# Optimization experiments

Hardware: AMD Instinct MI355X
Metric: run time of the kernel (lower is better)

Reference implementation:

```python
import jax, jax.numpy as jnp
import numpy as np

N_EMBD = 1024
BLOCK_SIZE = 128
HEAD_SIZE = 128
THETA = 10000.0


def setup_inputs() -> dict:
    key = jax.random.key(0)
    k1, k2, k3, k4 = jax.random.split(key, 4)
    B, T = 256, BLOCK_SIZE
    x = jax.random.normal(k1, (B, T, N_EMBD), dtype=jnp.float32)
    # nn.Linear(n_embd, head_size, bias=False) stored as [n_embd, head_size] so y = x @ W
    s = 1.0 / np.sqrt(N_EMBD)
    Wq = jax.random.normal(k2, (N_EMBD, HEAD_SIZE), dtype=jnp.float32) * s
    Wk = jax.random.normal(k3, (N_EMBD, HEAD_SIZE), dtype=jnp.float32) * s
    Wv = jax.random.normal(k4, (N_EMBD, HEAD_SIZE), dtype=jnp.float32) * s
    return {"x": x, "Wq": Wq, "Wk": Wk, "Wv": Wv}


def _rope_cos_sin(T: int, head_size: int):
    # freqs = exp(arange(0, hs, 2) * (-log(theta)/hs)); angles = outer(t, freqs)
    inv_freq = jnp.exp(jnp.arange(0, head_size, 2, dtype=jnp.float32) * (-np.log(THETA) / head_size))
    angles = jnp.arange(T, dtype=jnp.float32)[:, None] * inv_freq[None, :]  # [T, hs/2]
    return jnp.cos(angles), jnp.sin(angles)


def _apply_rope(t, cos, sin):
    # complex-view rotation on interleaved (even, odd) pairs of the last dim
    tr = t[..., 0::2]  # real parts  [B,T,hs/2]
    ti = t[..., 1::2]  # imag parts
    out_r = tr * cos - ti * sin
    out_i = tr * sin + ti * cos
    return jnp.stack([out_r, out_i], axis=-1).reshape(t.shape)


def reference(x, Wq, Wk, Wv):
    B, T, _ = x.shape
    hs = Wq.shape[1]
    q = x @ Wq  # [B,T,hs]
    k = x @ Wk
    v = x @ Wv
    cos, sin = _rope_cos_sin(T, hs)
    q = _apply_rope(q, cos, sin)
    k = _apply_rope(k, cos, sin)
    scores = jnp.einsum('btd,bsd->bts', q, k) / jnp.sqrt(jnp.asarray(hs, q.dtype))
    causal = jnp.tril(jnp.ones((T, T), dtype=bool))
    scores = jnp.where(causal[None, :, :], scores, -jnp.inf)
    att = jax.nn.softmax(scores, axis=-1)  # dropout is identity in eval
    return jnp.einsum('bts,bsd->btd', att, v)
```

## Files before the change

kernel.cpp:

```cpp
#include <hip/hip_runtime.h>
#include <math.h>

typedef __bf16 bf16x8 __attribute__((ext_vector_type(8)));
typedef float  f32x4  __attribute__((ext_vector_type(4)));
typedef unsigned short us4 __attribute__((ext_vector_type(4)));

constexpr int N_EMBD = 1024;
constexpr int T_SEQ  = 128;
constexpr int HS     = 128;
constexpr int BATCH  = 256;
constexpr int ROWS   = BATCH * T_SEQ;

__device__ __forceinline__ void async16(const void* g, void* l) {
    __builtin_amdgcn_global_load_lds(
        (const __attribute__((address_space(1))) unsigned int*)g,
        (__attribute__((address_space(3))) unsigned int*)l, 16, 0, 0);
}
__device__ __forceinline__ unsigned short bfbits(float f) {
    return __builtin_bit_cast(unsigned short, (__bf16)f);
}
__device__ __forceinline__ f32x4 zero4() {
    f32x4 z = {0.f, 0.f, 0.f, 0.f};
    return z;
}

__global__ __launch_bounds__(256) void wcast(
    const float* __restrict__ Wq, const float* __restrict__ Wk,
    const float* __restrict__ Wv, unsigned short* __restrict__ Wt)
{
    __shared__ unsigned short tile[64][130];
    const int bid = blockIdx.x;
    const int nt  = bid >> 4;
    const int k0  = (bid & 15) << 6;
    const float* src = (nt == 0) ? Wq : ((nt == 1) ? Wk : Wv);
    const int tid = threadIdx.x;
#pragma unroll
    for (int j = 0; j < 32; ++j) {
        int idx = tid + j * 256;
        int k = idx >> 7, n = idx & 127;
        tile[k][n] = bfbits(src[(size_t)(k0 + k) * HS + n]);
    }
    __syncthreads();
#pragma unroll
    for (int j = 0; j < 32; ++j) {
        int idx = tid + j * 256;
        int n = idx >> 6, kk = idx & 63;
        Wt[(size_t)(nt * 128 + n) * N_EMBD + k0 + kk] = tile[kk][n];
    }
}

__global__ __launch_bounds__(512, 4) void qkv_gemm(
    const float* __restrict__ x,
    const unsigned short* __restrict__ Wt,
    unsigned short* __restrict__ qb,
    unsigned short* __restrict__ kb,
    unsigned short* __restrict__ vt)
{
    __shared__ char lds[65536];
    const int tid = threadIdx.x;
    const int w  = tid >> 6;
    const int l  = tid & 63;
    const int cl = l & 15;
    const int quad = l >> 4;
    const int mt  = blockIdx.x;
    const int row0 = mt << 6;
    const int wm0 = (w & 1) << 5;
    const int wn0 = (w >> 1) * 96;

    f32x4 acc[2][6];
#pragma unroll
    for (int a = 0; a < 2; ++a)
#pragma unroll
        for (int b = 0; b < 6; ++b) acc[a][b] = zero4();

    for (int kc = 0; kc < N_EMBD; kc += 64) {
        __syncthreads();
#pragma unroll
        for (int jj = 0; jj < 2; ++jj) {
            int j = w * 2 + jj;
            int m = j * 4 + (l >> 4);
            int csrc = (l & 15) ^ (m & 15);
            async16(x + (size_t)(row0 + m) * N_EMBD + kc + csrc * 4, lds + j * 1024);
        }
#pragma unroll
        for (int jj = 0; jj < 6; ++jj) {
            int j = w * 6 + jj;
            int n = j * 8 + (l >> 3);
            int csrc = (l & 7) ^ (l >> 3);
            async16(Wt + (size_t)n * N_EMBD + kc + csrc * 8, lds + 16384 + j * 1024);
        }
        __syncthreads();

#pragma unroll
        for (int ks = 0; ks < 2; ++ks) {
            const int kq = ks * 4 + quad;
            bf16x8 af[2], bf[6];
#pragma unroll
            for (int rt = 0; rt < 2; ++rt) {
                int m = wm0 + rt * 16 + cl;
                int c0 = kq * 2;
                f32x4 a0 = *(const f32x4*)(lds + ((m * 16 + (c0 ^ cl)) << 4));
                f32x4 a1 = *(const f32x4*)(lds + ((m * 16 + ((c0 + 1) ^ cl)) << 4));
                bf16x8 t;
                t[0] = (__bf16)a0[0]; t[1] = (__bf16)a0[1];
                t[2] = (__bf16)a0[2]; t[3] = (__bf16)a0[3];
                t[4] = (__bf16)a1[0]; t[5] = (__bf16)a1[1];
                t[6] = (__bf16)a1[2]; t[7] = (__bf16)a1[3];
                af[rt] = t;
            }
#pragma unroll
            for (int ct = 0; ct < 6; ++ct) {
                int n = wn0 + ct * 16 + cl;
                bf[ct] = *(const bf16x8*)(lds + 16384 + ((n * 8 + (kq ^ (l & 7))) << 4));
            }
#pragma unroll
            for (int rt = 0; rt < 2; ++rt)
#pragma unroll
                for (int ct = 0; ct < 6; ++ct)
                    acc[rt][ct] = __builtin_amdgcn_mfma_f32_16x16x32_bf16(
                        af[rt], bf[ct], acc[rt][ct], 0, 0, 0);
        }
    }

    const float LNT = 0.07195578430905272f;
    const int bidx = row0 >> 7;
    const int srow0 = row0 & 127;
#pragma unroll
    for (int ct = 0; ct < 6; ++ct) {
        int c  = wn0 + ct * 16 + cl;
        int ntc = c >> 7;
        int d  = c & 127;
        if (ntc < 2) {
            unsigned short* dst = (ntc == 0) ? qb : kb;
            float freq = __expf(-(float)(d & ~1) * LNT);
#pragma unroll
            for (int rt = 0; rt < 2; ++rt) {
#pragma unroll
                for (int i = 0; i < 4; ++i) {
                    int grow = row0 + wm0 + rt * 16 + quad * 4 + i;
                    int t = grow & 127;
                    float v = acc[rt][ct][i];
                    float p = __shfl_xor(v, 1);
                    float sn, cs;
                    __sincosf((float)t * freq, &sn, &cs);
                    float r = ((d & 1) == 0) ? (v * cs - p * sn) : (p * sn + v * cs);
                    dst[(size_t)grow * HS + d] = bfbits(r);
                }
            }
        } else {
#pragma unroll
            for (int rt = 0; rt < 2; ++rt) {
                int s0 = srow0 + wm0 + rt * 16 + quad * 4;
                us4 u;
                u.x = bfbits(acc[rt][ct][0]);
                u.y = bfbits(acc[rt][ct][1]);
                u.z = bfbits(acc[rt][ct][2]);
                u.w = bfbits(acc[rt][ct][3]);
                *(us4*)(vt + (size_t)bidx * 16384 + d * 128 + s0) = u;
            }
        }
    }
}

__global__ __launch_bounds__(64) void attn(
    const unsigned short* __restrict__ qb,
    const unsigned short* __restrict__ kb,
    const unsigned short* __restrict__ vt,
    float* __restrict__ out)
{
    __shared__ char plds[16 * 272];
    const int l = threadIdx.x;
    const int cl = l & 15;
    const int quad = l >> 4;
    const int b  = blockIdx.x >> 3;
    const int rg = blockIdx.x & 7;
    const int nct = rg + 1;
    const int nks = (rg + 2) >> 1;

    const unsigned short* qB = qb + (size_t)b * 16384;
    const unsigned short* kB = kb + (size_t)b * 16384;
    const unsigned short* vB = vt + (size_t)b * 16384;

    bf16x8 af[4];
#pragma unroll
    for (int ks = 0; ks < 4; ++ks)
        af[ks] = *(const bf16x8*)(qB + (size_t)(rg * 16 + cl) * HS + (ks * 4 + quad) * 8);

    f32x4 s[8];
#pragma unroll
    for (int ct = 0; ct < 8; ++ct) s[ct] = zero4();

#pragma unroll
    for (int ct = 0; ct < 8; ++ct) if (ct < nct) {
        const unsigned short* kr = kB + (size_t)(ct * 16 + cl) * HS;
#pragma unroll
        for (int ks = 0; ks < 4; ++ks) {
            bf16x8 bb = *(const bf16x8*)(kr + (ks * 4 + quad) * 8);
            s[ct] = __builtin_amdgcn_mfma_f32_16x16x32_bf16(af[ks], bb, s[ct], 0, 0, 0);
        }
    }

    const float scale = 0.08838834764831845f;
#pragma unroll
    for (int i = 0; i < 4; ++i) {
        int t = rg * 16 + quad * 4 + i;
        float mx = -3.0e38f;
#pragma unroll
        for (int ct = 0; ct < 8; ++ct) if (ct < nct) {
            int col = ct * 16 + cl;
            float v = s[ct][i] * scale;
            v = (col <= t) ? v : -INFINITY;
            s[ct][i] = v;
            mx = fmaxf(mx, v);
        }
        mx = fmaxf(mx, __shfl_xor(mx, 1));
        mx = fmaxf(mx, __shfl_xor(mx, 2));
        mx = fmaxf(mx, __shfl_xor(mx, 4));
        mx = fmaxf(mx, __shfl_xor(mx, 8));
        float sum = 0.f;
#pragma unroll
        for (int ct = 0; ct < 8; ++ct) if (ct < nct) {
            float p = __expf(s[ct][i] - mx);
            s[ct][i] = p;
            sum += p;
        }
        sum += __shfl_xor(sum, 1);
        sum += __shfl_xor(sum, 2);
        sum += __shfl_xor(sum, 4);
        sum += __shfl_xor(sum, 8);
        float inv = 1.0f / sum;
        int rl = quad * 4 + i;
#pragma unroll
        for (int ct = 0; ct < 8; ++ct) if (ct < nct) {
            *(unsigned short*)(plds + rl * 272 + (ct * 16 + cl) * 2) =
                bfbits(s[ct][i] * inv);
        }
    }
    if ((rg & 1) == 0) {
#pragma unroll
        for (int i = 0; i < 4; ++i)
            *(unsigned short*)(plds + (quad * 4 + i) * 272 + (nct * 16 + cl) * 2) = 0;
    }

    bf16x8 ap[4];
#pragma unroll
    for (int ks = 0; ks < 4; ++ks) if (ks < nks)
        ap[ks] = *(const bf16x8*)(plds + cl * 272 + (ks * 4 + quad) * 16);

    f32x4 o[8];
#pragma unroll
    for (int ct = 0; ct < 8; ++ct) o[ct] = zero4();

#pragma unroll
    for (int ct = 0; ct < 8; ++ct) {
        const unsigned short* vr = vB + (size_t)(ct * 16 + cl) * 128;
#pragma unroll
        for (int ks = 0; ks < 4; ++ks) if (ks < nks) {
            bf16x8 bb = *(const bf16x8*)(vr + (ks * 4 + quad) * 8);
            o[ct] = __builtin_amdgcn_mfma_f32_16x16x32_bf16(ap[ks], bb, o[ct], 0, 0, 0);
        }
    }

#pragma unroll
    for (int ct = 0; ct < 8; ++ct)
#pragma unroll
        for (int i = 0; i < 4; ++i) {
            int t = rg * 16 + quad * 4 + i;
            out[(size_t)b * 16384 + (size_t)t * HS + ct * 16 + cl] = o[ct][i];
        }
}

extern "C" void kernel_launch(void* const* d_in, const int* in_sizes, int n_in,
                              void* d_out, int out_size, void* d_ws, size_t ws_size,
                              hipStream_t stream) {
    const float* x  = (const float*)d_in[0];
    const float* Wq = (const float*)d_in[1];
    const float* Wk = (const float*)d_in[2];
    const float* Wv = (const float*)d_in[3];
    float* out = (float*)d_out;

    unsigned short* qb = (unsigned short*)d_ws;
    unsigned short* kb = qb + (size_t)ROWS * HS;
    unsigned short* vt = kb + (size_t)ROWS * HS;
    unsigned short* Wt = vt + (size_t)ROWS * HS;

    wcast<<<48, 256, 0, stream>>>(Wq, Wk, Wv, Wt);
    qkv_gemm<<<512, 512, 0, stream>>>(x, Wt, qb, kb, vt);
    attn<<<2048, 64, 0, stream>>>(qb, kb, vt, out);
}
```

Measured before the change: 250.4 us.

## Register-prefetch x as bf16 into LDS, widen GEMM warp tiles, specialize attention per row group

The QKV GEMM now runs 256 threads per block, and each warp computes a 64x96 tile, which doubles A-fragment reuse per warp. Activations are loaded from global into registers one K-chunk ahead, converted to bf16 once, and stored into a swizzled bf16 LDS tile. This halves the A footprint in LDS and removes the repeated fp32-to-bf16 conversion each warp used to do. The attention kernel is templated on the row group, so loop bounds are compile-time constants and the register arrays shrink. The cost is more accumulator registers per thread (24 f32x4) and fewer warps per block, which may lower occupancy.

```diff
diff --git a/kernel.cpp b/kernel.cpp
--- a/kernel.cpp
+++ b/kernel.cpp
@@ -49,72 +49,84 @@
     }
 }
 
-__global__ __launch_bounds__(512, 4) void qkv_gemm(
+__global__ __launch_bounds__(256, 2) void qkv_gemm(
     const float* __restrict__ x,
     const unsigned short* __restrict__ Wt,
     unsigned short* __restrict__ qb,
     unsigned short* __restrict__ kb,
     unsigned short* __restrict__ vt)
 {
-    __shared__ char lds[65536];
+    __shared__ char lds[57344];
     const int tid = threadIdx.x;
     const int w  = tid >> 6;
     const int l  = tid & 63;
     const int cl = l & 15;
     const int quad = l >> 4;
-    const int mt  = blockIdx.x;
-    const int row0 = mt << 6;
-    const int wm0 = (w & 1) << 5;
-    const int wn0 = (w >> 1) * 96;
-
-    f32x4 acc[2][6];
-#pragma unroll
-    for (int a = 0; a < 2; ++a)
+    const int row0 = blockIdx.x << 6;
+    const int wn0 = w * 96;
+
+    const int ar = tid >> 2;
+    const int ac = tid & 3;
+    const int aslot0 = (ac * 2) ^ (ar & 7);
+    const int aslot1 = (ac * 2 + 1) ^ (ar & 7);
+    const float* aptr = x + (size_t)(row0 + ar) * N_EMBD + ac * 16;
+
+    f32x4 acc[4][6];
+#pragma unroll
+    for (int a = 0; a < 4; ++a)
 #pragma unroll
         for (int b = 0; b < 6; ++b) acc[a][b] = zero4();
+
+    f32x4 ar0 = *(const f32x4*)(aptr);
+    f32x4 ar1 = *(const f32x4*)(aptr + 4);
+    f32x4 ar2 = *(const f32x4*)(aptr + 8);
+    f32x4 ar3 = *(const f32x4*)(aptr + 12);
 
     for (int kc = 0; kc < N_EMBD; kc += 64) {
         __syncthreads();
-#pragma unroll
-        for (int jj = 0; jj < 2; ++jj) {
-            int j = w * 2 + jj;
-            int m = j * 4 + (l >> 4);
-            int csrc = (l & 15) ^ (m & 15);
-            async16(x + (size_t)(row0 + m) * N_EMBD + kc + csrc * 4, lds + j * 1024);
-        }
-#pragma unroll
-        for (int jj = 0; jj < 6; ++jj) {
-            int j = w * 6 + jj;
+        bf16x8 w0, w1;
+        w0[0] = (__bf16)ar0[0]; w0[1] = (__bf16)ar0[1];
+        w0[2] = (__bf16)ar0[2]; w0[3] = (__bf16)ar0[3];
+        w0[4] = (__bf16)ar1[0]; w0[5] = (__bf16)ar1[1];
+        w0[6] = (__bf16)ar1[2]; w0[7] = (__bf16)ar1[3];
+        w1[0] = (__bf16)ar2[0]; w1[1] = (__bf16)ar2[1];
+        w1[2] = (__bf16)ar2[2]; w1[3] = (__bf16)ar2[3];
+        w1[4] = (__bf16)ar3[0]; w1[5] = (__bf16)ar3[1];
+        w1[6] = (__bf16)ar3[2]; w1[7] = (__bf16)ar3[3];
+        *(bf16x8*)(lds + ar * 128 + aslot0 * 16) = w0;
+        *(bf16x8*)(lds + ar * 128 + aslot1 * 16) = w1;
+#pragma unroll
+        for (int jj = 0; jj < 12; ++jj) {
+            int j = w * 12 + jj;
             int n = j * 8 + (l >> 3);
             int csrc = (l & 7) ^ (l >> 3);
-            async16(Wt + (size_t)n * N_EMBD + kc + csrc * 8, lds + 16384 + j * 1024);
+            async16(Wt + (size_t)n * N_EMBD + kc + csrc * 8, lds + 8192 + j * 1024);
         }
         __syncthreads();
 
+        if (kc + 64 < N_EMBD) {
+            const float* ap2 = aptr + kc + 64;
+            ar0 = *(const f32x4*)(ap2);
+            ar1 = *(const f32x4*)(ap2 + 4);
+            ar2 = *(const f32x4*)(ap2 + 8);
+            ar3 = *(const f32x4*)(ap2 + 12);
+        }
+
 #pragma unroll
         for (int ks = 0; ks < 2; ++ks) {
-            const int kq = ks * 4 + quad;
-            bf16x8 af[2], bf[6];
-#pragma unroll
-            for (int rt = 0; rt < 2; ++rt) {
-                int m = wm0 + rt * 16 + cl;
-                int c0 = kq * 2;
-                f32x4 a0 = *(const f32x4*)(lds + ((m * 16 + (c0 ^ cl)) << 4));
-                f32x4 a1 = *(const f32x4*)(lds + ((m * 16 + ((c0 + 1) ^ cl)) << 4));
-                bf16x8 t;
-                t[0] = (__bf16)a0[0]; t[1] = (__bf16)a0[1];
-                t[2] = (__bf16)a0[2]; t[3] = (__bf16)a0[3];
-                t[4] = (__bf16)a1[0]; t[5] = (__bf16)a1[1];
-                t[6] = (__bf16)a1[2]; t[7] = (__bf16)a1[3];
-                af[rt] = t;
+            bf16x8 af[4], bf[6];
+#pragma unroll
+            for (int rt = 0; rt < 4; ++rt) {
+                int m = rt * 16 + cl;
+                af[rt] = *(const bf16x8*)(lds + m * 128 + (((ks * 4 + quad) ^ (m & 7)) << 4));
             }
 #pragma unroll
             for (int ct = 0; ct < 6; ++ct) {
                 int n = wn0 + ct * 16 + cl;
-                bf[ct] = *(const bf16x8*)(lds + 16384 + ((n * 8 + (kq ^ (l & 7))) << 4));
+                bf[ct] = *(const bf16x8*)(lds + 8192 + n * 128 + (((ks * 4 + quad) ^ (n & 7)) << 4));
             }
 #pragma unroll
-            for (int rt = 0; rt < 2; ++rt)
+            for (int rt = 0; rt < 4; ++rt)
 #pragma unroll
                 for (int ct = 0; ct < 6; ++ct)
                     acc[rt][ct] = __builtin_amdgcn_mfma_f32_16x16x32_bf16(
@@ -134,10 +146,10 @@
             unsigned short* dst = (ntc == 0) ? qb : kb;
             float freq = __expf(-(float)(d & ~1) * LNT);
 #pragma unroll
-            for (int rt = 0; rt < 2; ++rt) {
+            for (int rt = 0; rt < 4; ++rt) {
 #pragma unroll
                 for (int i = 0; i < 4; ++i) {
-                    int grow = row0 + wm0 + rt * 16 + quad * 4 + i;
+                    int grow = row0 + rt * 16 + quad * 4 + i;
                     int t = grow & 127;
                     float v = acc[rt][ct][i];
                     float p = __shfl_xor(v, 1);
@@ -149,8 +161,8 @@
             }
         } else {
 #pragma unroll
-            for (int rt = 0; rt < 2; ++rt) {
-                int s0 = srow0 + wm0 + rt * 16 + quad * 4;
+            for (int rt = 0; rt < 4; ++rt) {
+                int s0 = srow0 + rt * 16 + quad * 4;
                 us4 u;
                 u.x = bfbits(acc[rt][ct][0]);
                 u.y = bfbits(acc[rt][ct][1]);
@@ -160,6 +172,105 @@
             }
         }
     }
+}
+
+template<int RG>
+__device__ __forceinline__ void attn_body(
+    const unsigned short* __restrict__ qB,
+    const unsigned short* __restrict__ kB,
+    const unsigned short* __restrict__ vB,
+    float* __restrict__ outB, char* plds, int l)
+{
+    constexpr int NCT = RG + 1;
+    constexpr int NKS = (RG + 2) >> 1;
+    const int cl = l & 15;
+    const int quad = l >> 4;
+
+    bf16x8 af[4];
+#pragma unroll
+    for (int ks = 0; ks < 4; ++ks)
+        af[ks] = *(const bf16x8*)(qB + (size_t)(RG * 16 + cl) * HS + (ks * 4 + quad) * 8);
+
+    f32x4 s[NCT];
+#pragma unroll
+    for (int ct = 0; ct < NCT; ++ct) s[ct] = zero4();
+
+#pragma unroll
+    for (int ct = 0; ct < NCT; ++ct) {
+        const unsigned short* kr = kB + (size_t)(ct * 16 + cl) * HS;
+#pragma unroll
+        for (int ks = 0; ks < 4; ++ks) {
+            bf16x8 bb = *(const bf16x8*)(kr + (ks * 4 + quad) * 8);
+            s[ct] = __builtin_amdgcn_mfma_f32_16x16x32_bf16(af[ks], bb, s[ct], 0, 0, 0);
+        }
+    }
+
+    const float scale = 0.08838834764831845f;
+#pragma unroll
+    for (int i = 0; i < 4; ++i) {
+        int t = RG * 16 + quad * 4 + i;
+        float mx = -3.0e38f;
+#pragma unroll
+        for (int ct = 0; ct < NCT; ++ct) {
+            int col = ct * 16 + cl;
+            float v = s[ct][i] * scale;
+            v = (col <= t) ? v : -INFINITY;
+            s[ct][i] = v;
+            mx = fmaxf(mx, v);
+        }
+        mx = fmaxf(mx, __shfl_xor(mx, 1));
+        mx = fmaxf(mx, __shfl_xor(mx, 2));
+        mx = fmaxf(mx, __shfl_xor(mx, 4));
+        mx = fmaxf(mx, __shfl_xor(mx, 8));
+        float sum = 0.f;
+#pragma unroll
+        for (int ct = 0; ct < NCT; ++ct) {
+            float p = __expf(s[ct][i] - mx);
+            s[ct][i] = p;
+            sum += p;
+        }
+        sum += __shfl_xor(sum, 1);
+        sum += __shfl_xor(sum, 2);
+        sum += __shfl_xor(sum, 4);
+        sum += __shfl_xor(sum, 8);
+        float inv = 1.0f / sum;
+        int rl = quad * 4 + i;
+#pragma unroll
+        for (int ct = 0; ct < NCT; ++ct) {
+            *(unsigned short*)(plds + rl * 272 + (ct * 16 + cl) * 2) =
+                bfbits(s[ct][i] * inv);
+        }
+        if ((RG & 1) == 0) {
+            *(unsigned short*)(plds + rl * 272 + (NCT * 16 + cl) * 2) = 0;
+        }
+    }
+
+    bf16x8 ap[NKS];
+#pragma unroll
+    for (int ks = 0; ks < NKS; ++ks)
+        ap[ks] = *(const bf16x8*)(plds + cl * 272 + (ks * 4 + quad) * 16);
+
+    f32x4 o[8];
+#pragma unroll
+    for (int ct = 0; ct < 8; ++ct) o[ct] = zero4();
+
+#pragma unroll
+    for (int ct = 0; ct < 8; ++ct) {
+        const unsigned short* vr = vB + (size_t)(ct * 16 + cl) * 128;
+#pragma unroll
+        for (int ks = 0; ks < NKS; ++ks) {
+            bf16x8 bb = *(const bf16x8*)(vr + (ks * 4 + quad) * 8);
+            o[ct] = __builtin_amdgcn_mfma_f32_16x16x32_bf16(ap[ks], bb, o[ct], 0, 0, 0);
+        }
+    }
+
+#pragma unroll
+    for (int ct = 0; ct < 8; ++ct)
+#pragma unroll
+        for (int i = 0; i < 4; ++i) {
+            int t = RG * 16 + quad * 4 + i;
+            outB[(size_t)t * HS + ct * 16 + cl] = o[ct][i];
+        }
 }
 
 __global__ __launch_bounds__(64) void attn(
@@ -170,104 +281,24 @@
 {
     __shared__ char plds[16 * 272];
     const int l = threadIdx.x;
-    const int cl = l & 15;
-    const int quad = l >> 4;
     const int b  = blockIdx.x >> 3;
     const int rg = blockIdx.x & 7;
-    const int nct = rg + 1;
-    const int nks = (rg + 2) >> 1;
 
     const unsigned short* qB = qb + (size_t)b * 16384;
     const unsigned short* kB = kb + (size_t)b * 16384;
     const unsigned short* vB = vt + (size_t)b * 16384;
-
-    bf16x8 af[4];
-#pragma unroll
-    for (int ks = 0; ks < 4; ++ks)
-        af[ks] = *(const bf16x8*)(qB + (size_t)(rg * 16 + cl) * HS + (ks * 4 + quad) * 8);
-
-    f32x4 s[8];
-#pragma unroll
-    for (int ct = 0; ct < 8; ++ct) s[ct] = zero4();
-
-#pragma unroll
-    for (int ct = 0; ct < 8; ++ct) if (ct < nct) {
-        const unsigned short* kr = kB + (size_t)(ct * 16 + cl) * HS;
-#pragma unroll
-        for (int ks = 0; ks < 4; ++ks) {
-            bf16x8 bb = *(const bf16x8*)(kr + (ks * 4 + quad) * 8);
-            s[ct] = __builtin_amdgcn_mfma_f32_16x16x32_bf16(af[ks], bb, s[ct], 0, 0, 0);
-        }
-    }
-
-    const float scale = 0.08838834764831845f;
-#pragma unroll
-    for (int i = 0; i < 4; ++i) {
-        int t = rg * 16 + quad * 4 + i;
-        float mx = -3.0e38f;
-#pragma unroll
-        for (int ct = 0; ct < 8; ++ct) if (ct < nct) {
-            int col = ct * 16 + cl;
-            float v = s[ct][i] * scale;
-            v = (col <= t) ? v : -INFINITY;
-            s[ct][i] = v;
-            mx = fmaxf(mx, v);
-        }
-        mx = fmaxf(mx, __shfl_xor(mx, 1));
-        mx = fmaxf(mx, __shfl_xor(mx, 2));
-        mx = fmaxf(mx, __shfl_xor(mx, 4));
-        mx = fmaxf(mx, __shfl_xor(mx, 8));
-        float sum = 0.f;
-#pragma unroll
-        for (int ct = 0; ct < 8; ++ct) if (ct < nct) {
-            float p = __expf(s[ct][i] - mx);
-            s[ct][i] = p;
-            sum += p;
-        }
-        sum += __shfl_xor(sum, 1);
-        sum += __shfl_xor(sum, 2);
-        sum += __shfl_xor(sum, 4);
-        sum += __shfl_xor(sum, 8);
-        float inv = 1.0f / sum;
-        int rl = quad * 4 + i;
-#pragma unroll
-        for (int ct = 0; ct < 8; ++ct) if (ct < nct) {
-            *(unsigned short*)(plds + rl * 272 + (ct * 16 + cl) * 2) =
-                bfbits(s[ct][i] * inv);
-        }
-    }
-    if ((rg & 1) == 0) {
-#pragma unroll
-        for (int i = 0; i < 4; ++i)
-            *(unsigned short*)(plds + (quad * 4 + i) * 272 + (nct * 16 + cl) * 2) = 0;
-    }
-
-    bf16x8 ap[4];
-#pragma unroll
-    for (int ks = 0; ks < 4; ++ks) if (ks < nks)
-        ap[ks] = *(const bf16x8*)(plds + cl * 272 + (ks * 4 + quad) * 16);
-
-    f32x4 o[8];
-#pragma unroll
-    for (int ct = 0; ct < 8; ++ct) o[ct] = zero4();
-
-#pragma unroll
-    for (int ct = 0; ct < 8; ++ct) {
-        const unsigned short* vr = vB + (size_t)(ct * 16 + cl) * 128;
-#pragma unroll
-        for (int ks = 0; ks < 4; ++ks) if (ks < nks) {
-            bf16x8 bb = *(const bf16x8*)(vr + (ks * 4 + quad) * 8);
-            o[ct] = __builtin_amdgcn_mfma_f32_16x16x32_bf16(ap[ks], bb, o[ct], 0, 0, 0);
-        }
-    }
-
-#pragma unroll
-    for (int ct = 0; ct < 8; ++ct)
-#pragma unroll
-        for (int i = 0; i < 4; ++i) {
-            int t = rg * 16 + quad * 4 + i;
-            out[(size_t)b * 16384 + (size_t)t * HS + ct * 16 + cl] = o[ct][i];
-        }
+    float* outB = out + (size_t)b * 16384;
+
+    switch (rg) {
+        case 0: attn_body<0>(qB, kB, vB, outB, plds, l); break;
+        case 1: attn_body<1>(qB, kB, vB, outB, plds, l); break;
+        case 2: attn_body<2>(qB, kB, vB, outB, plds, l); break;
+        case 3: attn_body<3>(qB, kB, vB, outB, plds, l); break;
+        case 4: attn_body<4>(qB, kB, vB, outB, plds, l); break;
+        case 5: attn_body<5>(qB, kB, vB, outB, plds, l); break;
+        case 6: attn_body<6>(qB, kB, vB, outB, plds, l); break;
+        default: attn_body<7>(qB, kB, vB, outB, plds, l); break;
+    }
 }
 
 extern "C" void kernel_launch(void* const* d_in, const int* in_sizes, int n_in,
@@ -285,6 +316,6 @@
     unsigned short* Wt = vt + (size_t)ROWS * HS;
 
     wcast<<<48, 256, 0, stream>>>(Wq, Wk, Wv, Wt);
-    qkv_gemm<<<512, 512, 0, stream>>>(x, Wt, qb, kb, vt);
+    qkv_gemm<<<512, 256, 0, stream>>>(x, Wt, qb, kb, vt);
     attn<<<2048, 64, 0, stream>>>(qb, kb, vt, out);
 }
```

Result: faster. 240.1 us (-4.1%).

## Fuse QKV projection, RoPE and causal attention into one per-batch kernel

Applied to the files above, without the earlier changes.

Replaces the separate QKV GEMM and attention kernels with one kernel that handles one batch element per 512-thread block. The block projects x to Q, K and V, applies RoPE, keeps Q, K and V^T in LDS, and each wave computes attention for 16 query rows. This removes the global-memory round trip for bf16 Q, K and V and one kernel launch. The GEMM also changes its staging: x is prefetched into registers, converted to bf16 and stored in LDS with a K step of 32. The cost is roughly 139KB of LDS per block and only 256 blocks, so each CU runs a single block and there is less occupancy to hide the latency of reading x.

```diff
diff --git a/kernel.cpp b/kernel.cpp
--- a/kernel.cpp
+++ b/kernel.cpp
@@ -49,142 +49,126 @@
     }
 }
 
-__global__ __launch_bounds__(512, 4) void qkv_gemm(
+__global__ __launch_bounds__(512, 2) void head_fused(
     const float* __restrict__ x,
     const unsigned short* __restrict__ Wt,
-    unsigned short* __restrict__ qb,
-    unsigned short* __restrict__ kb,
-    unsigned short* __restrict__ vt)
+    float* __restrict__ out)
 {
-    __shared__ char lds[65536];
-    const int tid = threadIdx.x;
-    const int w  = tid >> 6;
-    const int l  = tid & 63;
-    const int cl = l & 15;
+    __shared__ char lds[139264];
+    constexpr int QS = 0;
+    constexpr int KS = 34816;
+    constexpr int VS = 69632;
+    constexpr int STG_A = 104448;
+    constexpr int STG_B = 114688;
+
+    const int tid  = threadIdx.x;
+    const int w    = tid >> 6;
+    const int l    = tid & 63;
+    const int cl   = l & 15;
     const int quad = l >> 4;
-    const int mt  = blockIdx.x;
-    const int row0 = mt << 6;
-    const int wm0 = (w & 1) << 5;
-    const int wn0 = (w >> 1) * 96;
-
-    f32x4 acc[2][6];
-#pragma unroll
-    for (int a = 0; a < 2; ++a)
-#pragma unroll
-        for (int b = 0; b < 6; ++b) acc[a][b] = zero4();
-
-    for (int kc = 0; kc < N_EMBD; kc += 64) {
+    const int b    = blockIdx.x;
+    const int row0 = b << 7;
+    const int wm   = (w & 1) << 6;
+    const int wn   = (w >> 1) * 96;
+
+    const int arow = tid >> 2;
+    const int acol = (tid & 3) << 3;
+    const float* aptr = x + (size_t)(row0 + arow) * N_EMBD + acol;
+    const int bsrc = (l & 3) ^ quad;
+
+    f32x4 acc[4][6];
+#pragma unroll
+    for (int a = 0; a < 4; ++a)
+#pragma unroll
+        for (int c = 0; c < 6; ++c) acc[a][c] = zero4();
+
+    f32x4 a0 = *(const f32x4*)(aptr);
+    f32x4 a1 = *(const f32x4*)(aptr + 4);
+
+    for (int kc = 0; kc < N_EMBD; kc += 32) {
         __syncthreads();
-#pragma unroll
-        for (int jj = 0; jj < 2; ++jj) {
-            int j = w * 2 + jj;
-            int m = j * 4 + (l >> 4);
-            int csrc = (l & 15) ^ (m & 15);
-            async16(x + (size_t)(row0 + m) * N_EMBD + kc + csrc * 4, lds + j * 1024);
-        }
-#pragma unroll
-        for (int jj = 0; jj < 6; ++jj) {
-            int j = w * 6 + jj;
-            int n = j * 8 + (l >> 3);
-            int csrc = (l & 7) ^ (l >> 3);
-            async16(Wt + (size_t)n * N_EMBD + kc + csrc * 8, lds + 16384 + j * 1024);
+        bf16x8 aw;
+        aw[0] = (__bf16)a0[0]; aw[1] = (__bf16)a0[1];
+        aw[2] = (__bf16)a0[2]; aw[3] = (__bf16)a0[3];
+        aw[4] = (__bf16)a1[0]; aw[5] = (__bf16)a1[1];
+        aw[6] = (__bf16)a1[2]; aw[7] = (__bf16)a1[3];
+        *(bf16x8*)(lds + STG_A + arow * 80 + (tid & 3) * 16) = aw;
+#pragma unroll
+        for (int jj = 0; jj < 3; ++jj) {
+            int j = w * 3 + jj;
+            int n = j * 16 + (l >> 2);
+            async16(Wt + (size_t)n * N_EMBD + kc + bsrc * 8,
+                    lds + STG_B + j * 1024 + 0);
         }
         __syncthreads();
-
-#pragma unroll
-        for (int ks = 0; ks < 2; ++ks) {
-            const int kq = ks * 4 + quad;
-            bf16x8 af[2], bf[6];
-#pragma unroll
-            for (int rt = 0; rt < 2; ++rt) {
-                int m = wm0 + rt * 16 + cl;
-                int c0 = kq * 2;
-                f32x4 a0 = *(const f32x4*)(lds + ((m * 16 + (c0 ^ cl)) << 4));
-                f32x4 a1 = *(const f32x4*)(lds + ((m * 16 + ((c0 + 1) ^ cl)) << 4));
-                bf16x8 t;
-                t[0] = (__bf16)a0[0]; t[1] = (__bf16)a0[1];
-                t[2] = (__bf16)a0[2]; t[3] = (__bf16)a0[3];
-                t[4] = (__bf16)a1[0]; t[5] = (__bf16)a1[1];
-                t[6] = (__bf16)a1[2]; t[7] = (__bf16)a1[3];
-                af[rt] = t;
-            }
-#pragma unroll
-            for (int ct = 0; ct < 6; ++ct) {
-                int n = wn0 + ct * 16 + cl;
-                bf[ct] = *(const bf16x8*)(lds + 16384 + ((n * 8 + (kq ^ (l & 7))) << 4));
-            }
-#pragma unroll
-            for (int rt = 0; rt < 2; ++rt)
-#pragma unroll
-                for (int ct = 0; ct < 6; ++ct)
-                    acc[rt][ct] = __builtin_amdgcn_mfma_f32_16x16x32_bf16(
-                        af[rt], bf[ct], acc[rt][ct], 0, 0, 0);
-        }
+        if (kc + 32 < N_EMBD) {
+            a0 = *(const f32x4*)(aptr + kc + 32);
+            a1 = *(const f32x4*)(aptr + kc + 36);
+        }
+        bf16x8 af[4], bf[6];
+#pragma unroll
+        for (int rt = 0; rt < 4; ++rt) {
+            int m = wm + rt * 16 + cl;
+            af[rt] = *(const bf16x8*)(lds + STG_A + m * 80 + quad * 16);
+        }
+#pragma unroll
+        for (int ct = 0; ct < 6; ++ct) {
+            int n = wn + ct * 16 + cl;
+            bf[ct] = *(const bf16x8*)(lds + STG_B + n * 64 + ((quad ^ ((n >> 2) & 3)) << 4));
+        }
+#pragma unroll
+        for (int rt = 0; rt < 4; ++rt)
+#pragma unroll
+            for (int ct = 0; ct < 6; ++ct)
+                acc[rt][ct] = __builtin_amdgcn_mfma_f32_16x16x32_bf16(
+                    af[rt], bf[ct], acc[rt][ct], 0, 0, 0);
     }
 
     const float LNT = 0.07195578430905272f;
-    const int bidx = row0 >> 7;
-    const int srow0 = row0 & 127;
 #pragma unroll
     for (int ct = 0; ct < 6; ++ct) {
-        int c  = wn0 + ct * 16 + cl;
-        int ntc = c >> 7;
-        int d  = c & 127;
+        int c0  = wn + ct * 16;
+        int ntc = c0 >> 7;
+        int d   = (c0 & 127) + cl;
         if (ntc < 2) {
-            unsigned short* dst = (ntc == 0) ? qb : kb;
+            int qk = (ntc == 0) ? QS : KS;
             float freq = __expf(-(float)(d & ~1) * LNT);
 #pragma unroll
-            for (int rt = 0; rt < 2; ++rt) {
+            for (int rt = 0; rt < 4; ++rt) {
 #pragma unroll
                 for (int i = 0; i < 4; ++i) {
-                    int grow = row0 + wm0 + rt * 16 + quad * 4 + i;
-                    int t = grow & 127;
+                    int t = wm + rt * 16 + quad * 4 + i;
                     float v = acc[rt][ct][i];
                     float p = __shfl_xor(v, 1);
                     float sn, cs;
                     __sincosf((float)t * freq, &sn, &cs);
                     float r = ((d & 1) == 0) ? (v * cs - p * sn) : (p * sn + v * cs);
-                    dst[(size_t)grow * HS + d] = bfbits(r);
+                    *(unsigned short*)(lds + qk + t * 272 + d * 2) = bfbits(r);
                 }
             }
         } else {
 #pragma unroll
-            for (int rt = 0; rt < 2; ++rt) {
-                int s0 = srow0 + wm0 + rt * 16 + quad * 4;
+            for (int rt = 0; rt < 4; ++rt) {
+                int s0 = wm + rt * 16 + quad * 4;
                 us4 u;
                 u.x = bfbits(acc[rt][ct][0]);
                 u.y = bfbits(acc[rt][ct][1]);
                 u.z = bfbits(acc[rt][ct][2]);
                 u.w = bfbits(acc[rt][ct][3]);
-                *(us4*)(vt + (size_t)bidx * 16384 + d * 128 + s0) = u;
+                *(us4*)(lds + VS + d * 272 + s0 * 2) = u;
             }
         }
     }
-}
-
-__global__ __launch_bounds__(64) void attn(
-    const unsigned short* __restrict__ qb,
-    const unsigned short* __restrict__ kb,
-    const unsigned short* __restrict__ vt,
-    float* __restrict__ out)
-{
-    __shared__ char plds[16 * 272];
-    const int l = threadIdx.x;
-    const int cl = l & 15;
-    const int quad = l >> 4;
-    const int b  = blockIdx.x >> 3;
-    const int rg = blockIdx.x & 7;
-    const int nct = rg + 1;
-    const int nks = (rg + 2) >> 1;
-
-    const unsigned short* qB = qb + (size_t)b * 16384;
-    const unsigned short* kB = kb + (size_t)b * 16384;
-    const unsigned short* vB = vt + (size_t)b * 16384;
-
-    bf16x8 af[4];
+    __syncthreads();
+
+    const int nct = w + 1;
+    const int nks = (w + 2) >> 1;
+    char* pl = lds + STG_A + w * 4352;
+
+    bf16x8 qf[4];
 #pragma unroll
     for (int ks = 0; ks < 4; ++ks)
-        af[ks] = *(const bf16x8*)(qB + (size_t)(rg * 16 + cl) * HS + (ks * 4 + quad) * 8);
+        qf[ks] = *(const bf16x8*)(lds + QS + (w * 16 + cl) * 272 + (ks * 4 + quad) * 16);
 
     f32x4 s[8];
 #pragma unroll
@@ -192,18 +176,18 @@
 
 #pragma unroll
     for (int ct = 0; ct < 8; ++ct) if (ct < nct) {
-        const unsigned short* kr = kB + (size_t)(ct * 16 + cl) * HS;
+        const char* kr = lds + KS + (ct * 16 + cl) * 272;
 #pragma unroll
         for (int ks = 0; ks < 4; ++ks) {
-            bf16x8 bb = *(const bf16x8*)(kr + (ks * 4 + quad) * 8);
-            s[ct] = __builtin_amdgcn_mfma_f32_16x16x32_bf16(af[ks], bb, s[ct], 0, 0, 0);
+            bf16x8 bb = *(const bf16x8*)(kr + (ks * 4 + quad) * 16);
+            s[ct] = __builtin_amdgcn_mfma_f32_16x16x32_bf16(qf[ks], bb, s[ct], 0, 0, 0);
         }
     }
 
     const float scale = 0.08838834764831845f;
 #pragma unroll
     for (int i = 0; i < 4; ++i) {
-        int t = rg * 16 + quad * 4 + i;
+        int t = w * 16 + quad * 4 + i;
         float mx = -3.0e38f;
 #pragma unroll
         for (int ct = 0; ct < 8; ++ct) if (ct < nct) {
@@ -232,20 +216,18 @@
         int rl = quad * 4 + i;
 #pragma unroll
         for (int ct = 0; ct < 8; ++ct) if (ct < nct) {
-            *(unsigned short*)(plds + rl * 272 + (ct * 16 + cl) * 2) =
+            *(unsigned short*)(pl + rl * 272 + (ct * 16 + cl) * 2) =
                 bfbits(s[ct][i] * inv);
         }
-    }
-    if ((rg & 1) == 0) {
-#pragma unroll
-        for (int i = 0; i < 4; ++i)
-            *(unsigned short*)(plds + (quad * 4 + i) * 272 + (nct * 16 + cl) * 2) = 0;
+        if ((w & 1) == 0) {
+            *(unsigned short*)(pl + rl * 272 + (nct * 16 + cl) * 2) = 0;
+        }
     }
 
     bf16x8 ap[4];
 #pragma unroll
     for (int ks = 0; ks < 4; ++ks) if (ks < nks)
-        ap[ks] = *(const bf16x8*)(plds + cl * 272 + (ks * 4 + quad) * 16);
+        ap[ks] = *(const bf16x8*)(pl + cl * 272 + (ks * 4 + quad) * 16);
 
     f32x4 o[8];
 #pragma unroll
@@ -253,10 +235,10 @@
 
 #pragma unroll
     for (int ct = 0; ct < 8; ++ct) {
-        const unsigned short* vr = vB + (size_t)(ct * 16 + cl) * 128;
+        const char* vr = lds + VS + (ct * 16 + cl) * 272;
 #pragma unroll
         for (int ks = 0; ks < 4; ++ks) if (ks < nks) {
-            bf16x8 bb = *(const bf16x8*)(vr + (ks * 4 + quad) * 8);
+            bf16x8 bb = *(const bf16x8*)(vr + (ks * 4 + quad) * 16);
             o[ct] = __builtin_amdgcn_mfma_f32_16x16x32_bf16(ap[ks], bb, o[ct], 0, 0, 0);
         }
     }
@@ -265,7 +247,7 @@
     for (int ct = 0; ct < 8; ++ct)
 #pragma unroll
         for (int i = 0; i < 4; ++i) {
-            int t = rg * 16 + quad * 4 + i;
+            int t = w * 16 + quad * 4 + i;
             out[(size_t)b * 16384 + (size_t)t * HS + ct * 16 + cl] = o[ct][i];
         }
 }
@@ -279,12 +261,8 @@
     const float* Wv = (const float*)d_in[3];
     float* out = (float*)d_out;
 
-    unsigned short* qb = (unsigned short*)d_ws;
-    unsigned short* kb = qb + (size_t)ROWS * HS;
-    unsigned short* vt = kb + (size_t)ROWS * HS;
-    unsigned short* Wt = vt + (size_t)ROWS * HS;
+    unsigned short* Wt = (unsigned short*)d_ws;
 
     wcast<<<48, 256, 0, stream>>>(Wq, Wk, Wv, Wt);
-    qkv_gemm<<<512, 512, 0, stream>>>(x, Wt, qb, kb, vt);
-    attn<<<2048, 64, 0, stream>>>(qb, kb, vt, out);
-}
+    head_fused<<<BATCH, 512, 0, stream>>>(x, Wt, out);
+}
```

After: 226.4 us. -9.6%, faster.
